# Kernel tuning notes

Hardware: AMD Instinct MI355X
Metric: run time of the kernel (lower is better)

## Reference

```python
import jax, jax.numpy as jnp
import numpy as np

KH, KW = 3, 3
PAD, STRIDE = 1, 1
KD = 3  # depth kernel extent; extended with one zero slice -> 4 indices


def _unfold(x, pad, stride):
    # x: (B, C, H, W) -> (B, C, KH*KW, oH, oW), patches ordered row-major like F.unfold
    B, C, H, W = x.shape
    xp = jnp.pad(x, ((0, 0), (0, 0), (pad, pad), (pad, pad)))
    oH = (H + 2 * pad - KH) // stride + 1
    oW = (W + 2 * pad - KW) // stride + 1
    pats = [xp[:, :, i:i + (oH - 1) * stride + 1:stride, j:j + (oW - 1) * stride + 1:stride]
            for i in range(KH) for j in range(KW)]
    return jnp.stack(pats, axis=2)


def setup_inputs() -> dict:
    key = jax.random.key(0)
    k1, k2, k3 = jax.random.split(key, 3)
    features = jax.random.normal(k1, (4, 16, 512, 512), dtype=jnp.float32)
    depth = jax.random.randint(k2, (4, 512, 512), 0, 8, dtype=jnp.int32)
    weight = jax.random.normal(k3, (32, 16, 3, 3, 3), dtype=jnp.float32) * 0.05
    return {"features": features, "depth": depth, "weight": weight}


def reference(features, depth, weight):
    oC, iC = weight.shape[0], weight.shape[1]
    # unfolded input patches: (B, iC, 9, oH, oW)
    patches = _unfold(features, PAD, STRIDE)
    # unfolded depth: (B, 9, oH, oW); padding fills with depth 0 (matches F.unfold)
    dpat = _unfold(depth[:, None, :, :].astype(jnp.int32), PAD, STRIDE)[:, 0]
    center = dpat[:, KH * KW // 2][:, None]  # (B, 1, oH, oW)
    diff = dpat - center
    # diff < -1 or diff >= 1 -> select appended zero slice (index 3); else diff+1
    idx = jnp.where((diff < -1) | (diff >= 1), 3, diff + 1)  # (B, 9, oH, oW) in [0, 3]
    onehot = jax.nn.one_hot(idx, KD + 1, dtype=features.dtype)  # (B, 9, oH, oW, 4)
    # extended weight with zero depth-slice: (oC, iC, 4, 9)
    ext_w = jnp.concatenate([weight, jnp.zeros_like(weight[:, :, :1])], axis=2)
    ext_w = ext_w.reshape(oC, iC, KD + 1, KH * KW)
    # per-pixel depth-gated 3x3x3 conv (bias is never added in the original op)
    out = jnp.einsum('oidk,bkhwd,bikhw->bohw', ext_w, onehot, patches)
    return out
```

## Files before the change

kernel.cpp:

```cpp
#include <hip/hip_runtime.h>
#include <hip/hip_bf16.h>


#define IC 16
#define OC 32
#define Hh 512
#define Ww 512
#define HW (Hh * Ww)
#define TW 256
#define TR 4
#define PXS 20
#define SENT (1 << 20)

typedef __attribute__((ext_vector_type(8))) short short8;
typedef __attribute__((ext_vector_type(4))) float float4v;
typedef __attribute__((ext_vector_type(2))) unsigned int uint2v;

__device__ __forceinline__ unsigned short f2bf(float x) {
    unsigned u = __float_as_uint(x);
    unsigned r = u + 0x7FFFu + ((u >> 16) & 1u);
    return (unsigned short)(r >> 16);
}

__device__ __forceinline__ unsigned packbf(float a, float b) {
    union { __hip_bfloat162 h2; unsigned u; } cv;
    cv.h2 = __float22bfloat162_rn(make_float2(a, b));
    return cv.u;
}

__global__ void prep_weights(const float* __restrict__ wgt,
                             unsigned short* __restrict__ wsA) {
    int e = blockIdx.x * 256 + threadIdx.x;
    if (e >= 9 * 2 * 64 * 8) return;
    int j    = e & 7;
    int lane = (e >> 3) & 63;
    int mt   = (e >> 9) & 1;
    int c    = e >> 10;
    int oc = mt * 16 + (lane & 15);
    int kk = ((lane >> 4) << 3) + j;
    wsA[e] = f2bf(wgt[oc * 432 + (kk >> 1) * 27 + (kk & 1) * 9 + c]);
}

__global__ __launch_bounds__(512, 2) void depconv_fused(
    const float* __restrict__ feat,
    const int*   __restrict__ depth,
    const unsigned short* __restrict__ wsA,
    float*       __restrict__ out)
{
    __shared__ unsigned short ftile[TR + 2][TW + 2][PXS];
    __shared__ int            dtile[TR + 2][TW + 2];

    const int tid = threadIdx.x;

    const int bid = blockIdx.x;
    const int wg  = (bid & 7) * (1024 / 8) + (bid >> 3);

    const int b      = wg >> 8;
    const int rowblk = (wg >> 1) & 127;
    const int colblk = wg & 1;
    const int h0     = rowblk * TR;
    const int wstart = colblk * TW;

    {
        const int h8 = tid >> 8;
        const int xl = tid & 255;
        const int x  = wstart - 1 + xl;
        const bool xin = (unsigned)x < (unsigned)Ww;
        const int xc = x < 0 ? 0 : (x > Ww - 1 ? Ww - 1 : x);
        const int xt  = wstart - 1 + 256 + xl;
        const bool xtin = (unsigned)xt < (unsigned)Ww;
        const int xct = xt > Ww - 1 ? Ww - 1 : xt;
        const float* fb  = feat + (size_t)(b * IC + 8 * h8) * HW;
        const int*   dbp = depth + (b << 18);
#pragma unroll
        for (int r = 0; r < 6; ++r) {
            const int y = h0 - 1 + r;
            const bool yin = (unsigned)y < (unsigned)Hh;
            const int yc = y < 0 ? 0 : (y > Hh - 1 ? Hh - 1 : y);
            const float* fpl = fb + (size_t)yc * Ww;
            if (h8 == 0) {
                dtile[r][xl] = (yin & xin) ? dbp[yc * Ww + xc] : SENT;
                if (xl < 2)
                    dtile[r][256 + xl] = (yin & xtin) ? dbp[yc * Ww + xct] : SENT;
            }
            unsigned pk[4];
#pragma unroll
            for (int i = 0; i < 4; ++i)
                pk[i] = packbf(fpl[(size_t)(2 * i) * HW + xc],
                               fpl[(size_t)(2 * i + 1) * HW + xc]);
            unsigned short* wp = &ftile[r][xl][h8 * 8];
            *(uint2v*)wp       = (uint2v){pk[0], pk[1]};
            *(uint2v*)(wp + 4) = (uint2v){pk[2], pk[3]};
            if (xl < 2) {
                unsigned qk[4];
#pragma unroll
                for (int i = 0; i < 4; ++i)
                    qk[i] = packbf(fpl[(size_t)(2 * i) * HW + xct],
                                   fpl[(size_t)(2 * i + 1) * HW + xct]);
                unsigned short* wq = &ftile[r][256 + xl][h8 * 8];
                *(uint2v*)wq       = (uint2v){qk[0], qk[1]};
                *(uint2v*)(wq + 4) = (uint2v){qk[2], qk[3]};
            }
        }
    }

    const int lane = tid & 63;
    short8 afrag[9][2];
    {
        const short8* ap = (const short8*)wsA;
#pragma unroll
        for (int c = 0; c < 9; ++c) {
            afrag[c][0] = ap[(c * 2 + 0) * 64 + lane];
            afrag[c][1] = ap[(c * 2 + 1) * 64 + lane];
        }
    }
    __syncthreads();

    const int wv   = tid >> 6;
    const int g    = lane >> 4;
    const int n    = lane & 15;
    const int rr   = wv >> 1;
    const int h    = h0 + rr;
    const int xoff = (wv & 1) * 128;

    float* opb = out + ((size_t)(b * OC) << 18) + (size_t)h * Ww;

    for (int it = 0; it < 8; ++it) {
        const int xb = xoff + it * 16 + n;
        const int w  = wstart + xb;
        const int dc = dtile[rr + 1][xb + 1];

        float4v acc0 = {0.f, 0.f, 0.f, 0.f};
        float4v acc1 = {0.f, 0.f, 0.f, 0.f};

#pragma unroll
        for (int t = 0; t < 9; ++t) {
            const int kh = t / 3, kw = t % 3;
            unsigned mm;
            if (t == 4) {
                mm = 0xffff0000u;
            } else {
                const int diff = dtile[rr + kh][xb + kw] - dc;
                mm = (diff == 0) ? 0xffff0000u : ((diff == -1) ? 0x0000ffffu : 0u);
            }
            const uint2v pr = *(const uint2v*)(&ftile[rr + kh][xb + kw][g << 2]);
            union { short8 s; unsigned u[4]; } bf;
            bf.u[0] = __builtin_amdgcn_perm(0u, pr.x, 0x01000100u) & mm;
            bf.u[1] = __builtin_amdgcn_perm(0u, pr.x, 0x03020302u) & mm;
            bf.u[2] = __builtin_amdgcn_perm(0u, pr.y, 0x01000100u) & mm;
            bf.u[3] = __builtin_amdgcn_perm(0u, pr.y, 0x03020302u) & mm;

            __builtin_amdgcn_s_setprio(1);
            acc0 = __builtin_amdgcn_mfma_f32_16x16x32_bf16(afrag[t][0], bf.s, acc0, 0, 0, 0);
            acc1 = __builtin_amdgcn_mfma_f32_16x16x32_bf16(afrag[t][1], bf.s, acc1, 0, 0, 0);
            __builtin_amdgcn_s_setprio(0);
        }

        const int rbase = g * 4;
        float* op = opb + w;
#pragma unroll
        for (int r = 0; r < 4; ++r) {
            op[(size_t)(rbase + r) * HW]      = acc0[r];
            op[(size_t)(16 + rbase + r) * HW] = acc1[r];
        }
    }
}

extern "C" void kernel_launch(void* const* d_in, const int* in_sizes, int n_in,
                              void* d_out, int out_size, void* d_ws, size_t ws_size,
                              hipStream_t stream) {
    const float* feat  = (const float*)d_in[0];
    const int*   depth = (const int*)d_in[1];
    const float* wgt   = (const float*)d_in[2];
    float* out = (float*)d_out;

    unsigned short* wsA = (unsigned short*)d_ws;

    prep_weights<<<36, 256, 0, stream>>>(wgt, wsA);
    depconv_fused<<<1024, 512, 0, stream>>>(feat, depth, wsA, out);
}
```

Baseline: 214.0 us.

## Swizzle feature tile in LDS and shrink depth tile to 16-bit

The padded 20-element-per-pixel shared-memory feature tile becomes a dense 16-element-per-pixel layout. The 4-element channel groups are XOR-swizzled by pixel index, and per-kw column pointers are precomputed, all to cut LDS bank conflicts on the 8-byte fragment reads feeding the MFMAs. The depth tile is stored as unsigned short with a smaller sentinel, which halves its shared-memory footprint. The s_setprio hints around the MFMA pair are removed, which may change how waves interleave.

```diff
diff --git a/kernel.cpp b/kernel.cpp
--- a/kernel.cpp
+++ b/kernel.cpp
@@ -9,8 +9,8 @@
 #define HW (Hh * Ww)
 #define TW 256
 #define TR 4
-#define PXS 20
-#define SENT (1 << 20)
+#define ROWSH 4128
+#define SENT 0x1000
 
 typedef __attribute__((ext_vector_type(8))) short short8;
 typedef __attribute__((ext_vector_type(4))) float float4v;
@@ -47,8 +47,8 @@
     const unsigned short* __restrict__ wsA,
     float*       __restrict__ out)
 {
-    __shared__ unsigned short ftile[TR + 2][TW + 2][PXS];
-    __shared__ int            dtile[TR + 2][TW + 2];
+    __shared__ unsigned short ftile[6 * ROWSH];
+    __shared__ unsigned short dtile[6][TW + 2];
 
     const int tid = threadIdx.x;
 
@@ -70,6 +70,7 @@
         const int xt  = wstart - 1 + 256 + xl;
         const bool xtin = (unsigned)xt < (unsigned)Ww;
         const int xct = xt > Ww - 1 ? Ww - 1 : xt;
+        const int qx = (xl >> 2) & 3;
         const float* fb  = feat + (size_t)(b * IC + 8 * h8) * HW;
         const int*   dbp = depth + (b << 18);
 #pragma unroll
@@ -79,27 +80,28 @@
             const int yc = y < 0 ? 0 : (y > Hh - 1 ? Hh - 1 : y);
             const float* fpl = fb + (size_t)yc * Ww;
             if (h8 == 0) {
-                dtile[r][xl] = (yin & xin) ? dbp[yc * Ww + xc] : SENT;
+                dtile[r][xl] = (yin & xin) ? (unsigned short)dbp[yc * Ww + xc] : (unsigned short)SENT;
                 if (xl < 2)
-                    dtile[r][256 + xl] = (yin & xtin) ? dbp[yc * Ww + xct] : SENT;
+                    dtile[r][256 + xl] = (yin & xtin) ? (unsigned short)dbp[yc * Ww + xct]
+                                                      : (unsigned short)SENT;
             }
             unsigned pk[4];
 #pragma unroll
             for (int i = 0; i < 4; ++i)
                 pk[i] = packbf(fpl[(size_t)(2 * i) * HW + xc],
                                fpl[(size_t)(2 * i + 1) * HW + xc]);
-            unsigned short* wp = &ftile[r][xl][h8 * 8];
-            *(uint2v*)wp       = (uint2v){pk[0], pk[1]};
-            *(uint2v*)(wp + 4) = (uint2v){pk[2], pk[3]};
+            unsigned short* wp = &ftile[r * ROWSH + xl * 16];
+            *(uint2v*)(wp + ((((2 * h8)     ) ^ qx) << 2)) = (uint2v){pk[0], pk[1]};
+            *(uint2v*)(wp + ((((2 * h8) + 1) ^ qx) << 2)) = (uint2v){pk[2], pk[3]};
             if (xl < 2) {
                 unsigned qk[4];
 #pragma unroll
                 for (int i = 0; i < 4; ++i)
                     qk[i] = packbf(fpl[(size_t)(2 * i) * HW + xct],
                                    fpl[(size_t)(2 * i + 1) * HW + xct]);
-                unsigned short* wq = &ftile[r][256 + xl][h8 * 8];
-                *(uint2v*)wq       = (uint2v){qk[0], qk[1]};
-                *(uint2v*)(wq + 4) = (uint2v){qk[2], qk[3]};
+                unsigned short* wq = &ftile[r * ROWSH + (256 + xl) * 16];
+                *(uint2v*)(wq + (((2 * h8)     ) << 2)) = (uint2v){qk[0], qk[1]};
+                *(uint2v*)(wq + (((2 * h8) + 1) << 2)) = (uint2v){qk[2], qk[3]};
             }
         }
     }
@@ -124,11 +126,20 @@
     const int xoff = (wv & 1) * 128;
 
     float* opb = out + ((size_t)(b * OC) << 18) + (size_t)h * Ww;
+    const unsigned short* frow0 = &ftile[rr * ROWSH];
 
     for (int it = 0; it < 8; ++it) {
         const int xb = xoff + it * 16 + n;
         const int w  = wstart + xb;
         const int dc = dtile[rr + 1][xb + 1];
+
+        const unsigned short* colp[3];
+#pragma unroll
+        for (int kw = 0; kw < 3; ++kw) {
+            const int px = xb + kw;
+            const int q  = (px >> 2) & 3;
+            colp[kw] = frow0 + px * 16 + ((g ^ q) << 2);
+        }
 
         float4v acc0 = {0.f, 0.f, 0.f, 0.f};
         float4v acc1 = {0.f, 0.f, 0.f, 0.f};
@@ -140,20 +151,18 @@
             if (t == 4) {
                 mm = 0xffff0000u;
             } else {
-                const int diff = dtile[rr + kh][xb + kw] - dc;
+                const int diff = (int)dtile[rr + kh][xb + kw] - dc;
                 mm = (diff == 0) ? 0xffff0000u : ((diff == -1) ? 0x0000ffffu : 0u);
             }
-            const uint2v pr = *(const uint2v*)(&ftile[rr + kh][xb + kw][g << 2]);
+            const uint2v pr = *(const uint2v*)(colp[kw] + kh * ROWSH);
             union { short8 s; unsigned u[4]; } bf;
             bf.u[0] = __builtin_amdgcn_perm(0u, pr.x, 0x01000100u) & mm;
             bf.u[1] = __builtin_amdgcn_perm(0u, pr.x, 0x03020302u) & mm;
             bf.u[2] = __builtin_amdgcn_perm(0u, pr.y, 0x01000100u) & mm;
             bf.u[3] = __builtin_amdgcn_perm(0u, pr.y, 0x03020302u) & mm;
 
-            __builtin_amdgcn_s_setprio(1);
             acc0 = __builtin_amdgcn_mfma_f32_16x16x32_bf16(afrag[t][0], bf.s, acc0, 0, 0, 0);
             acc1 = __builtin_amdgcn_mfma_f32_16x16x32_bf16(afrag[t][1], bf.s, acc1, 0, 0, 0);
-            __builtin_amdgcn_s_setprio(0);
         }
 
         const int rbase = g * 4;
```

Result: no change. 213.8 us (-0.1%).
